# Optimization experiments

Measured on AMD Instinct MI355X. Metric: run time of the kernel, lower is better.

## Reference

```python
import jax, jax.numpy as jnp
import numpy as np

DIM = 1024
NUM_HEADS = 16
HEAD_DIM = DIM // NUM_HEADS
SCALE = HEAD_DIM ** -0.5


def setup_inputs() -> dict:
    key = jax.random.key(0)
    ks = jax.random.split(key, 8)
    B, N, L = 2, 256, 8192
    x = jax.random.normal(ks[0], (B, N, DIM), dtype=jnp.float32)
    past_k = jax.random.normal(ks[1], (B, NUM_HEADS, L, HEAD_DIM), dtype=jnp.float32)
    past_v = jax.random.normal(ks[2], (B, NUM_HEADS, L, HEAD_DIM), dtype=jnp.float32)
    s = DIM ** -0.5
    w_qkv = jax.random.normal(ks[3], (DIM, 3 * DIM), dtype=jnp.float32) * s
    b_qkv = jnp.zeros((3 * DIM,), dtype=jnp.float32)
    w_proj = jax.random.normal(ks[4], (DIM, DIM), dtype=jnp.float32) * s
    b_proj = jnp.zeros((DIM,), dtype=jnp.float32)
    return {"x": x, "past_k": past_k, "past_v": past_v,
            "w_qkv": w_qkv, "b_qkv": b_qkv, "w_proj": w_proj, "b_proj": b_proj}


def reference(x, past_k, past_v, w_qkv, b_qkv, w_proj, b_proj):
    B, N, C = x.shape
    qkv = (x @ w_qkv + b_qkv).reshape(B, N, 3, NUM_HEADS, HEAD_DIM)
    qkv = jnp.transpose(qkv, (2, 0, 3, 1, 4))
    q, k_new, v_new = qkv[0], qkv[1], qkv[2]
    # Streaming KV cache append (torch.cat along seq dim)
    k_all = jnp.concatenate([past_k, k_new], axis=-2)  # [B, H, L+N, D]
    v_all = jnp.concatenate([past_v, v_new], axis=-2)
    # Scaled dot-product attention (non-causal full attention over cache)
    scores = jnp.einsum("bhnd,bhld->bhnl", q, k_all) * SCALE
    attn = jax.nn.softmax(scores, axis=-1)
    out = jnp.einsum("bhnl,bhld->bhnd", attn, v_all)  # [B, H, N, D]
    out = jnp.transpose(out, (0, 2, 1, 3)).reshape(B, N, C)
    return out @ w_proj + b_proj
```

## Files before the change

### kernel.cpp

```cpp
#include <hip/hip_runtime.h>
#include <hip/hip_bf16.h>


#define BB 2
#define NH 16
#define NQ 256
#define HD 64
#define DIMC 1024
#define LPAST 8192
#define TOTK 8448
#define NSPLIT 16

typedef __attribute__((ext_vector_type(8))) short short8;
typedef __attribute__((ext_vector_type(4))) float f32x4;
typedef __attribute__((ext_vector_type(16))) float f32x16;
typedef __attribute__((ext_vector_type(4))) int int4v;

#define DEVI static __device__ __forceinline__

DEVI float exp2g(float x) { return __builtin_amdgcn_exp2f(x); }

DEVI int cvtpk(float lo, float hi) {
  int r;
  asm("v_cvt_pk_bf16_f32 %0, %1, %2" : "=v"(r) : "v"(lo), "v"(hi));
  return r;
}
DEVI short f2bf(float f) {
  union { float f; unsigned u; } v; v.f = f;
  unsigned r = v.u + 0x7FFFu + ((v.u >> 16) & 1u);
  return (short)(r >> 16);
}

template<int MODE>
__global__ __launch_bounds__(256, 2) void gemm_k(
    const float* __restrict__ A, const float* __restrict__ Bm,
    const float* __restrict__ bias, float* __restrict__ Cout,
    short* __restrict__ qbuf, float* __restrict__ knew, float* __restrict__ vnew,
    int M, int Nn, int K)
{
  __shared__ alignas(16) short As[64][72];
  __shared__ alignas(16) short Bs[64][72];
  const int tid = threadIdx.x;
  const int lane = tid & 63, wave = tid >> 6;
  const int nblk = Nn >> 6;
  const int bi = blockIdx.x / nblk, bj = blockIdx.x % nblk;
  const int wm = wave >> 1, wn = wave & 1;
  const int g = lane >> 4, l16 = lane & 15;
  f32x4 acc[2][2] = {};
  const int r = tid >> 2, q4 = (tid & 3) << 4;

  for (int k0 = 0; k0 < K; k0 += 64) {
    const float* pa = A + (size_t)(bi * 64 + r) * K + (k0 + q4);
    float4 a0 = ((const float4*)pa)[0];
    float4 a1 = ((const float4*)pa)[1];
    float4 a2 = ((const float4*)pa)[2];
    float4 a3 = ((const float4*)pa)[3];
    const float* pb = Bm + (size_t)(k0 + r) * Nn + (bj * 64 + q4);
    float4 b0 = ((const float4*)pb)[0];
    float4 b1 = ((const float4*)pb)[1];
    float4 b2 = ((const float4*)pb)[2];
    float4 b3 = ((const float4*)pb)[3];
    __syncthreads();
    {
      int4v p0 = {cvtpk(a0.x,a0.y), cvtpk(a0.z,a0.w), cvtpk(a1.x,a1.y), cvtpk(a1.z,a1.w)};
      int4v p1 = {cvtpk(a2.x,a2.y), cvtpk(a2.z,a2.w), cvtpk(a3.x,a3.y), cvtpk(a3.z,a3.w)};
      *(int4v*)&As[r][q4]     = p0;
      *(int4v*)&As[r][q4 + 8] = p1;
    }
    Bs[q4+ 0][r] = f2bf(b0.x); Bs[q4+ 1][r] = f2bf(b0.y);
    Bs[q4+ 2][r] = f2bf(b0.z); Bs[q4+ 3][r] = f2bf(b0.w);
    Bs[q4+ 4][r] = f2bf(b1.x); Bs[q4+ 5][r] = f2bf(b1.y);
    Bs[q4+ 6][r] = f2bf(b1.z); Bs[q4+ 7][r] = f2bf(b1.w);
    Bs[q4+ 8][r] = f2bf(b2.x); Bs[q4+ 9][r] = f2bf(b2.y);
    Bs[q4+10][r] = f2bf(b2.z); Bs[q4+11][r] = f2bf(b2.w);
    Bs[q4+12][r] = f2bf(b3.x); Bs[q4+13][r] = f2bf(b3.y);
    Bs[q4+14][r] = f2bf(b3.z); Bs[q4+15][r] = f2bf(b3.w);
    __syncthreads();
    #pragma unroll
    for (int kf = 0; kf < 2; ++kf) {
      short8 af[2], bfv[2];
      #pragma unroll
      for (int mt = 0; mt < 2; ++mt)
        af[mt] = *(const short8*)&As[wm*32 + mt*16 + l16][kf*32 + g*8];
      #pragma unroll
      for (int nt = 0; nt < 2; ++nt)
        bfv[nt] = *(const short8*)&Bs[wn*32 + nt*16 + l16][kf*32 + g*8];
      #pragma unroll
      for (int mt = 0; mt < 2; ++mt)
        #pragma unroll
        for (int nt = 0; nt < 2; ++nt)
          acc[mt][nt] = __builtin_amdgcn_mfma_f32_16x16x32_bf16(
              af[mt], bfv[nt], acc[mt][nt], 0, 0, 0);
    }
  }

  #pragma unroll
  for (int mt = 0; mt < 2; ++mt)
    #pragma unroll
    for (int nt = 0; nt < 2; ++nt)
      #pragma unroll
      for (int rg = 0; rg < 4; ++rg) {
        int row = bi*64 + wm*32 + mt*16 + g*4 + rg;
        int col = bj*64 + wn*32 + nt*16 + l16;
        float val = acc[mt][nt][rg] + bias[col];
        if (MODE == 0) {
          Cout[(size_t)row * Nn + col] = val;
        } else {
          int which = col >> 10, cc = col & 1023;
          int h = cc >> 6, d = cc & 63;
          int b = row >> 8, n = row & 255;
          size_t idx = (((size_t)(b*NH + h))*NQ + n)*HD + d;
          if (which == 0)      qbuf[idx] = f2bf(val * 0.180336878f);
          else if (which == 1) knew[idx] = val;
          else                 vnew[idx] = val;
        }
      }
}

__global__ __launch_bounds__(512, 2) void attn_k(
    const short* __restrict__ qbuf, const float* __restrict__ pastk,
    const float* __restrict__ pastv, const float* __restrict__ knew,
    const float* __restrict__ vnew, float* __restrict__ opart,
    float* __restrict__ mbuf, float* __restrict__ lbuf)
{
  __shared__ alignas(16) short Kt[2][64][64];
  __shared__ alignas(16) short Vt[2][64][64];
  const int tid = threadIdx.x;
  const int lane = tid & 63, wave = tid >> 6;
  const int h = lane >> 5, c = lane & 31;
  const int s = blockIdx.x & (NSPLIT - 1), bh = blockIdx.x / NSPLIT;
  const int kr = tid >> 3, kc8 = (tid & 7) << 3;
  const int vp = tid >> 4, vd = tid & 15;
  const int vpi = ((vp>>4)<<5) | (((vp>>2)&1)<<4) | (((vp>>1)&1)<<3)
                | (((vp>>3)&1)<<2) | ((vp&1)<<1);
  const int vsw = vpi ^ ((vd & 7) << 3);
  const int csw = (c & 7) << 3;

  short8 qf[4];
  #pragma unroll
  for (int dk = 0; dk < 4; ++dk)
    qf[dk] = *(const short8*)(qbuf + ((size_t)bh*NQ + wave*32 + c)*HD + 16*dk + 8*h);

  f32x16 acc[2] = {};
  float m_s = -INFINITY, l_s = 0.f;

  const int first  = 8*s + (s < 4 ? s : 4);
  const int nsteps = 8 + (s < 4 ? 1 : 0);

  float kfl[8], vlo[4], vhi[4];
  auto load = [&](int step) {
    const float* kp = (step < 128)
        ? pastk + ((size_t)bh*LPAST + step*64 + kr)*HD + kc8
        : knew  + ((size_t)bh*NQ + (step - 128)*64 + kr)*HD + kc8;
    *(float4*)&kfl[0] = *(const float4*)kp;
    *(float4*)&kfl[4] = *(const float4*)(kp + 4);
    const float* vq = (step < 128)
        ? pastv + ((size_t)bh*LPAST + step*64 + 2*vp)*HD + vd
        : vnew  + ((size_t)bh*NQ + (step - 128)*64 + 2*vp)*HD + vd;
    #pragma unroll
    for (int j = 0; j < 4; ++j) { vlo[j] = vq[16*j]; vhi[j] = vq[HD + 16*j]; }
  };
  auto stage = [&](int b) {
    int4v kp4 = {cvtpk(kfl[0],kfl[1]), cvtpk(kfl[2],kfl[3]),
                 cvtpk(kfl[4],kfl[5]), cvtpk(kfl[6],kfl[7])};
    *(int4v*)&Kt[b][kr][kc8 ^ ((kr & 7) << 3)] = kp4;
    #pragma unroll
    for (int j = 0; j < 4; ++j)
      *(int*)&Vt[b][vd + 16*j][vsw] = cvtpk(vlo[j], vhi[j]);
  };

  load(first);
  stage(0);
  if (nsteps > 1) load(first + 1);
  __syncthreads();

  for (int it = 0; it < nsteps; ++it) {
    const int cur = it & 1;

    f32x16 sv0 = {}, sv1 = {};
    __builtin_amdgcn_s_setprio(1);
    #pragma unroll
    for (int dk = 0; dk < 4; ++dk) {
      short8 k0 = *(const short8*)&Kt[cur][c][(16*dk + 8*h) ^ csw];
      sv0 = __builtin_amdgcn_mfma_f32_32x32x16_bf16(k0, qf[dk], sv0, 0,0,0);
    }
    #pragma unroll
    for (int dk = 0; dk < 4; ++dk) {
      short8 k1 = *(const short8*)&Kt[cur][32 + c][(16*dk + 8*h) ^ csw];
      sv1 = __builtin_amdgcn_mfma_f32_32x32x16_bf16(k1, qf[dk], sv1, 0,0,0);
    }
    __builtin_amdgcn_s_setprio(0);

    float t16[16];
    #pragma unroll
    for (int r = 0; r < 16; ++r) t16[r] = fmaxf(sv0[r], sv1[r]);
    #pragma unroll
    for (int w = 8; w >= 1; w >>= 1)
      #pragma unroll
      for (int r = 0; r < w; ++r) t16[r] = fmaxf(t16[r], t16[r + w]);
    float mx = fmaxf(t16[0], __shfl_xor(t16[0], 32));

    if (!__all(mx <= m_s + 8.f)) {
      float mn = fmaxf(m_s, mx);
      float al = exp2g(m_s - mn);
      l_s *= al;
      #pragma unroll
      for (int r = 0; r < 16; ++r) {
        float a = __shfl(al, (r&3) + 8*(r>>2) + 4*h);
        acc[0][r] *= a; acc[1][r] *= a;
      }
      m_s = mn;
    }
    float ss = 0.f;
    #pragma unroll
    for (int r = 0; r < 16; ++r) {
      float p0 = exp2g(sv0[r] - m_s); sv0[r] = p0;
      float p1 = exp2g(sv1[r] - m_s); sv1[r] = p1;
      ss += p0 + p1;
    }
    ss += __shfl_xor(ss, 32);
    l_s += ss;

    short8 pa[4];
    #pragma unroll
    for (int kc = 0; kc < 4; ++kc) {
      int4v w;
      #pragma unroll
      for (int jd = 0; jd < 4; ++jd) {
        int r0 = 8*(jd>>1) + 4*(kc&1) + 2*(jd&1);
        w[jd] = (kc < 2) ? cvtpk(sv0[r0], sv0[r0+1])
                         : cvtpk(sv1[r0], sv1[r0+1]);
      }
      pa[kc] = __builtin_bit_cast(short8, w);
    }

    __builtin_amdgcn_s_setprio(1);
    #pragma unroll
    for (int kc = 0; kc < 4; ++kc) {
      #pragma unroll
      for (int dt = 0; dt < 2; ++dt) {
        short8 vf = *(const short8*)&Vt[cur][32*dt + c][(16*kc + 8*h) ^ csw];
        acc[dt] = __builtin_amdgcn_mfma_f32_32x32x16_bf16(pa[kc], vf, acc[dt], 0,0,0);
      }
    }
    __builtin_amdgcn_s_setprio(0);

    if (it + 1 < nsteps) {
      stage(1 - cur);
      if (it + 2 < nsteps) load(first + it + 2);
      __syncthreads();
    }
  }

  size_t pbase = ((size_t)(bh * NSPLIT + s)) * NQ;
  #pragma unroll
  for (int dt = 0; dt < 2; ++dt)
    #pragma unroll
    for (int r = 0; r < 16; ++r) {
      int row = wave*32 + (r&3) + 8*(r>>2) + 4*h;
      opart[(pbase + row)*HD + 32*dt + c] = acc[dt][r];
    }
  if (lane < 32) {
    mbuf[pbase + wave*32 + c] = m_s;
    lbuf[pbase + wave*32 + c] = l_s;
  }
}

__global__ __launch_bounds__(256) void combine_k(
    const float* __restrict__ opart, const float* __restrict__ mbuf,
    const float* __restrict__ lbuf, float* __restrict__ attnout)
{
  const int lane = threadIdx.x & 63, wave = threadIdx.x >> 6;
  const int rid = blockIdx.x * 4 + wave;
  const int bh = rid >> 8, n = rid & 255;
  const int b = bh >> 4, h = bh & 15;
  float M = -INFINITY;
  float ms[NSPLIT], ls[NSPLIT];
  #pragma unroll
  for (int s = 0; s < NSPLIT; ++s) {
    size_t base = ((size_t)(bh * NSPLIT + s)) * NQ + n;
    ms[s] = mbuf[base]; ls[s] = lbuf[base];
    M = fmaxf(M, ms[s]);
  }
  float denom = 0.f, o = 0.f;
  #pragma unroll
  for (int s = 0; s < NSPLIT; ++s) {
    float w = exp2g(ms[s] - M);
    denom += w * ls[s];
    o += w * opart[(((size_t)(bh * NSPLIT + s)) * NQ + n) * HD + lane];
  }
  attnout[((size_t)(b * NQ + n)) * DIMC + h * HD + lane] = o / denom;
}

extern "C" void kernel_launch(void* const* d_in, const int* in_sizes, int n_in,
                              void* d_out, int out_size, void* d_ws, size_t ws_size,
                              hipStream_t stream)
{
  const float* x     = (const float*)d_in[0];
  const float* pastk = (const float*)d_in[1];
  const float* pastv = (const float*)d_in[2];
  const float* wqkv  = (const float*)d_in[3];
  const float* bqkv  = (const float*)d_in[4];
  const float* wproj = (const float*)d_in[5];
  const float* bproj = (const float*)d_in[6];
  float* out = (float*)d_out;
  char* ws = (char*)d_ws;

  size_t off = 0;
  short* qbuf   = (short*)(ws + off); off += (size_t)BB*NH*NQ*HD*2;
  float* knew   = (float*)(ws + off); off += (size_t)BB*NH*NQ*HD*4;
  float* vnew   = (float*)(ws + off); off += (size_t)BB*NH*NQ*HD*4;
  float* opart  = (float*)(ws + off); off += (size_t)BB*NH*NSPLIT*NQ*HD*4;
  float* mbuf   = (float*)(ws + off); off += (size_t)BB*NH*NSPLIT*NQ*4;
  float* lbuf   = (float*)(ws + off); off += (size_t)BB*NH*NSPLIT*NQ*4;
  float* attnout= (float*)(ws + off); off += (size_t)BB*NQ*DIMC*4;

  gemm_k<1><<<(512/64)*(3072/64), 256, 0, stream>>>(
      x, wqkv, bqkv, nullptr, qbuf, knew, vnew, 512, 3072, 1024);
  attn_k<<<BB*NH*NSPLIT, 512, 0, stream>>>(
      qbuf, pastk, pastv, knew, vnew, opart, mbuf, lbuf);
  combine_k<<<BB*NH*NQ/4, 256, 0, stream>>>(opart, mbuf, lbuf, attnout);
  gemm_k<0><<<(512/64)*(1024/64), 256, 0, stream>>>(
      attnout, wproj, bproj, out, nullptr, nullptr, nullptr, 512, 1024, 1024);
}
```

Measured before the change: 89.39 us.

## Overlap KV staging with softmax, vectorize V loads, defer row-sum shuffles

Result: no change. 90.33 us (+1.0%).

```diff
diff --git a/kernel.cpp b/kernel.cpp
--- a/kernel.cpp
+++ b/kernel.cpp
@@ -29,6 +29,10 @@
   union { float f; unsigned u; } v; v.f = f;
   unsigned r = v.u + 0x7FFFu + ((v.u >> 16) & 1u);
   return (short)(r >> 16);
+}
+DEVI void ldsbar() {
+  asm volatile("s_waitcnt lgkmcnt(0)" ::: "memory");
+  __builtin_amdgcn_s_barrier();
 }
 
 template<int MODE>
@@ -60,7 +64,7 @@
     float4 b1 = ((const float4*)pb)[1];
     float4 b2 = ((const float4*)pb)[2];
     float4 b3 = ((const float4*)pb)[3];
-    __syncthreads();
+    ldsbar();
     {
       int4v p0 = {cvtpk(a0.x,a0.y), cvtpk(a0.z,a0.w), cvtpk(a1.x,a1.y), cvtpk(a1.z,a1.w)};
       int4v p1 = {cvtpk(a2.x,a2.y), cvtpk(a2.z,a2.w), cvtpk(a3.x,a3.y), cvtpk(a3.z,a3.w)};
@@ -75,7 +79,7 @@
     Bs[q4+10][r] = f2bf(b2.z); Bs[q4+11][r] = f2bf(b2.w);
     Bs[q4+12][r] = f2bf(b3.x); Bs[q4+13][r] = f2bf(b3.y);
     Bs[q4+14][r] = f2bf(b3.z); Bs[q4+15][r] = f2bf(b3.w);
-    __syncthreads();
+    ldsbar();
     #pragma unroll
     for (int kf = 0; kf < 2; ++kf) {
       short8 af[2], bfv[2];
@@ -130,10 +134,9 @@
   const int h = lane >> 5, c = lane & 31;
   const int s = blockIdx.x & (NSPLIT - 1), bh = blockIdx.x / NSPLIT;
   const int kr = tid >> 3, kc8 = (tid & 7) << 3;
-  const int vp = tid >> 4, vd = tid & 15;
+  const int vp = tid >> 4, vd4 = (tid & 15) << 2;
   const int vpi = ((vp>>4)<<5) | (((vp>>2)&1)<<4) | (((vp>>1)&1)<<3)
                 | (((vp>>3)&1)<<2) | ((vp&1)<<1);
-  const int vsw = vpi ^ ((vd & 7) << 3);
   const int csw = (c & 7) << 3;
 
   short8 qf[4];
@@ -147,7 +150,8 @@
   const int first  = 8*s + (s < 4 ? s : 4);
   const int nsteps = 8 + (s < 4 ? 1 : 0);
 
-  float kfl[8], vlo[4], vhi[4];
+  float kfl[8];
+  float4 vA, vB;
   auto load = [&](int step) {
     const float* kp = (step < 128)
         ? pastk + ((size_t)bh*LPAST + step*64 + kr)*HD + kc8
@@ -155,24 +159,28 @@
     *(float4*)&kfl[0] = *(const float4*)kp;
     *(float4*)&kfl[4] = *(const float4*)(kp + 4);
     const float* vq = (step < 128)
-        ? pastv + ((size_t)bh*LPAST + step*64 + 2*vp)*HD + vd
-        : vnew  + ((size_t)bh*NQ + (step - 128)*64 + 2*vp)*HD + vd;
-    #pragma unroll
-    for (int j = 0; j < 4; ++j) { vlo[j] = vq[16*j]; vhi[j] = vq[HD + 16*j]; }
+        ? pastv + ((size_t)bh*LPAST + step*64 + 2*vp)*HD + vd4
+        : vnew  + ((size_t)bh*NQ + (step - 128)*64 + 2*vp)*HD + vd4;
+    vA = *(const float4*)vq;
+    vB = *(const float4*)(vq + HD);
   };
   auto stage = [&](int b) {
     int4v kp4 = {cvtpk(kfl[0],kfl[1]), cvtpk(kfl[2],kfl[3]),
                  cvtpk(kfl[4],kfl[5]), cvtpk(kfl[6],kfl[7])};
     *(int4v*)&Kt[b][kr][kc8 ^ ((kr & 7) << 3)] = kp4;
-    #pragma unroll
-    for (int j = 0; j < 4; ++j)
-      *(int*)&Vt[b][vd + 16*j][vsw] = cvtpk(vlo[j], vhi[j]);
+    const float* af = (const float*)&vA;
+    const float* cf = (const float*)&vB;
+    #pragma unroll
+    for (int i = 0; i < 4; ++i) {
+      int row = vd4 + i;
+      *(int*)&Vt[b][row][vpi ^ ((row & 7) << 3)] = cvtpk(af[i], cf[i]);
+    }
   };
 
   load(first);
   stage(0);
   if (nsteps > 1) load(first + 1);
-  __syncthreads();
+  ldsbar();
 
   for (int it = 0; it < nsteps; ++it) {
     const int cur = it & 1;
@@ -191,6 +199,11 @@
     }
     __builtin_amdgcn_s_setprio(0);
 
+    if (it + 1 < nsteps) {
+      stage(1 - cur);
+      if (it + 2 < nsteps) load(first + it + 2);
+    }
+
     float t16[16];
     #pragma unroll
     for (int r = 0; r < 16; ++r) t16[r] = fmaxf(sv0[r], sv1[r]);
@@ -198,9 +211,10 @@
     for (int w = 8; w >= 1; w >>= 1)
       #pragma unroll
       for (int r = 0; r < w; ++r) t16[r] = fmaxf(t16[r], t16[r + w]);
-    float mx = fmaxf(t16[0], __shfl_xor(t16[0], 32));
-
-    if (!__all(mx <= m_s + 8.f)) {
+    float mxh = t16[0];
+
+    if (!__all(mxh <= m_s + 8.f)) {
+      float mx = fmaxf(mxh, __shfl_xor(mxh, 32));
       float mn = fmaxf(m_s, mx);
       float al = exp2g(m_s - mn);
       l_s *= al;
@@ -218,7 +232,6 @@
       float p1 = exp2g(sv1[r] - m_s); sv1[r] = p1;
       ss += p0 + p1;
     }
-    ss += __shfl_xor(ss, 32);
     l_s += ss;
 
     short8 pa[4];
@@ -245,13 +258,10 @@
     }
     __builtin_amdgcn_s_setprio(0);
 
-    if (it + 1 < nsteps) {
-      stage(1 - cur);
-      if (it + 2 < nsteps) load(first + it + 2);
-      __syncthreads();
-    }
-  }
-
+    if (it + 1 < nsteps) ldsbar();
+  }
+
+  float l_tot = l_s + __shfl_xor(l_s, 32);
   size_t pbase = ((size_t)(bh * NSPLIT + s)) * NQ;
   #pragma unroll
   for (int dt = 0; dt < 2; ++dt)
@@ -262,7 +272,7 @@
     }
   if (lane < 32) {
     mbuf[pbase + wave*32 + c] = m_s;
-    lbuf[pbase + wave*32 + c] = l_s;
+    lbuf[pbase + wave*32 + c] = l_tot;
   }
 }
 
```
